# Optimization experiments

Measured on AMD Instinct MI355X. Metric: run time of the kernel, lower is better.

The kernel has to match this reference:

```python
import jax, jax.numpy as jnp
import numpy as np
from jax import lax

K = 3  # conv kernel size (causal)

def causal_conv1d(x, w, b):
    # x: [B, T, Cin], w: [K, Cin, Cout], b: [Cout]
    # TF 'causal' padding = pad left with (K-1) zeros.
    y = lax.conv_general_dilated(
        x, w,
        window_strides=(1,),
        padding=[(K - 1, 0)],
        dimension_numbers=("NWC", "WIO", "NWC"),
    )
    return y + b

def setup_inputs() -> dict:
    key = jax.random.key(0)
    ks = jax.random.split(key, 7)
    B, T, Cin, U = 8, 2048, 512, 512
    scale_in = 1.0 / np.sqrt(K * Cin)
    x = jax.random.normal(ks[0], (B, T, Cin), dtype=jnp.float32)
    Wq = jax.random.normal(ks[1], (K, Cin, U), dtype=jnp.float32) * scale_in
    Wk = jax.random.normal(ks[2], (K, Cin, U), dtype=jnp.float32) * scale_in
    Wv = jax.random.normal(ks[3], (K, Cin, U), dtype=jnp.float32) * scale_in
    bq = jnp.zeros((U,), dtype=jnp.float32)
    bk = jnp.zeros((U,), dtype=jnp.float32)
    bv = jnp.zeros((U,), dtype=jnp.float32)
    return {"x": x, "Wq": Wq, "bq": bq, "Wk": Wk, "bk": bk, "Wv": Wv, "bv": bv}

def reference(x, Wq, bq, Wk, bk, Wv, bv):
    # Self-attention path: query = key = value = x
    q = causal_conv1d(x, Wq, bq)   # [B, T, U]
    k = causal_conv1d(x, Wk, bk)   # [B, T, U]
    v = causal_conv1d(x, Wv, bv)   # [B, T, U]
    score = jnp.einsum("bqd,bkd->bqk", q, k)
    score = score / jnp.sqrt(jnp.asarray(v.shape[-1], dtype=score.dtype))
    # NOTE: faithful to source — softmax over axis=1 (the QUERY axis)
    score = jax.nn.softmax(score, axis=1)
    context = jnp.einsum("bqk,bkd->bqd", score, v)  # [B, T, U]
    return context
```

## Files before the change

### kernel.cpp

```cpp
#include <hip/hip_runtime.h>


#define B_   8
#define T_   2048
#define D_   512
#define KC_  1536
#define TPAD_ 2050

using short8   = __attribute__((ext_vector_type(8))) short;
using float4v  = __attribute__((ext_vector_type(4))) float;

__device__ __forceinline__ float bf2f(unsigned short b) {
  unsigned u = ((unsigned)b) << 16;
  float f; __builtin_memcpy(&f, &u, 4); return f;
}
__device__ __forceinline__ unsigned short f2bf(float f) {
  unsigned u; __builtin_memcpy(&u, &f, 4);
  u += 0x7fffu + ((u >> 16) & 1u);
  return (unsigned short)(u >> 16);
}

__device__ __forceinline__ void gld16(const void* g, void* l) {
  __builtin_amdgcn_global_load_lds((__attribute__((address_space(1))) void*)g,
                                   (__attribute__((address_space(3))) void*)l,
                                   16, 0, 0);
}

__device__ __forceinline__ float4v mfma16(short8 a, short8 b, float4v c) {
  return __builtin_amdgcn_mfma_f32_16x16x32_bf16(a, b, c, 0, 0, 0);
}

__global__ __launch_bounds__(256) void prep_x(const float* __restrict__ x,
                                              unsigned short* __restrict__ xpad) {
  const int b = blockIdx.y;
  const int i = (blockIdx.x * 256 + threadIdx.x) * 4;
  const int t = i >> 9;
  unsigned short* dst = xpad + (size_t)b * (TPAD_ * D_) + i;
  if (t < 2) {
    dst[0] = 0; dst[1] = 0; dst[2] = 0; dst[3] = 0;
  } else {
    const float* sp = x + ((size_t)b * T_ + (t - 2)) * D_ + (i & 511);
    float4v v = *(const float4v*)sp;
    dst[0] = f2bf(v[0]); dst[1] = f2bf(v[1]); dst[2] = f2bf(v[2]); dst[3] = f2bf(v[3]);
  }
}

__global__ __launch_bounds__(256) void transpose_w3(const float* __restrict__ Wq,
                                                    const float* __restrict__ Wk,
                                                    const float* __restrict__ Wv,
                                                    unsigned short* __restrict__ Wt,
                                                    const float* __restrict__ bq,
                                                    const float* __restrict__ bk,
                                                    const float* __restrict__ bv,
                                                    float* __restrict__ bcat) {
  __shared__ unsigned short tile[64][65];
  const float* s = (blockIdx.z == 0) ? Wq : (blockIdx.z == 1) ? Wk : Wv;
  unsigned short* d = Wt + (size_t)blockIdx.z * D_ * KC_;
  const int r0 = blockIdx.x * 64, c0 = blockIdx.y * 64;
  const int tc = threadIdx.x & 63, tg = threadIdx.x >> 6;
  if (blockIdx.x == 0 && blockIdx.y == 0) {
    const float* bsrc = (blockIdx.z == 0) ? bq : (blockIdx.z == 1) ? bk : bv;
    bcat[blockIdx.z * 512 + threadIdx.x] = bsrc[threadIdx.x];
    bcat[blockIdx.z * 512 + 256 + threadIdx.x] = bsrc[256 + threadIdx.x];
  }
#pragma unroll
  for (int i = 0; i < 16; i++) {
    const int r = i * 4 + tg;
    tile[r][tc] = f2bf(s[(size_t)(r0 + r) * D_ + (c0 + tc)]);
  }
  __syncthreads();
#pragma unroll
  for (int i = 0; i < 16; i++) {
    const int rr = i * 4 + tg;
    d[(size_t)(c0 + rr) * KC_ + (r0 + tc)] = tile[tc][rr];
  }
}

__global__ __launch_bounds__(256) void transpose_v(const unsigned short* __restrict__ src,
                                                   unsigned short* __restrict__ dst) {
  __shared__ unsigned short tile[64][65];
  const unsigned short* s = src + (size_t)blockIdx.z * T_ * KC_;
  unsigned short* d = dst + (size_t)blockIdx.z * D_ * T_;
  const int r0 = blockIdx.x * 64, c0 = blockIdx.y * 64;
  const int tc = threadIdx.x & 63, tg = threadIdx.x >> 6;
#pragma unroll
  for (int i = 0; i < 16; i++) {
    const int r = i * 4 + tg;
    tile[r][tc] = s[(size_t)(r0 + r) * KC_ + (c0 + tc)];
  }
  __syncthreads();
#pragma unroll
  for (int i = 0; i < 16; i++) {
    const int rr = i * 4 + tg;
    d[(size_t)(c0 + rr) * T_ + (r0 + tc)] = tile[tc][rr];
  }
}

__global__ __launch_bounds__(256) void scale_vt2(unsigned short* __restrict__ Vt,
                                                 long long sVz,
                                                 const float* __restrict__ pl,
                                                 long long sPz) {
  const size_t z = blockIdx.z;
  unsigned short* Vb = Vt + z * (size_t)sVz;
  const float* Lz = pl + z * (size_t)sPz;
  const int k0 = threadIdx.x * 8;
  float4v a = *(const float4v*)(Lz + k0);
  float4v b = *(const float4v*)(Lz + k0 + 4);
  float inv[8];
#pragma unroll
  for (int j = 0; j < 4; j++) { inv[j] = 1.f / a[j]; inv[4 + j] = 1.f / b[j]; }
  const int d0 = blockIdx.x * 8;
#pragma unroll
  for (int r = 0; r < 8; r++) {
    unsigned short* p = Vb + (size_t)(d0 + r) * T_ + k0;
    short8 v = *(const short8*)p;
    short8 o;
#pragma unroll
    for (int j = 0; j < 8; j++)
      o[j] = (short)f2bf(bf2f((unsigned short)v[j]) * inv[j]);
    *(short8*)p = o;
  }
}


#define RD_A(MH, BUF)                                                        \
  {                                                                          \
    const unsigned short* p_ =                                               \
        lds + (BUF) * 8192 + aoff + (MH) * (HFA * 1024);                     \
    _Pragma("unroll") for (int f_ = 0; f_ < HFA; ++f_) {                     \
      afr[MH][f_][0] = *(const short8*)(p_ + f_ * 1024 + q0);                \
      afr[MH][f_][1] = *(const short8*)(p_ + f_ * 1024 + q1);                \
    }                                                                        \
  }

#define RD_B(NH, BUF)                                                        \
  {                                                                          \
    const unsigned short* p_ =                                               \
        lds + 16384 + (BUF) * BLD + boff + (NH) * (HFB * 1024);              \
    _Pragma("unroll") for (int f_ = 0; f_ < HFB; ++f_) {                     \
      bfr[NH][f_][0] = *(const short8*)(p_ + f_ * 1024 + q0);                \
      bfr[NH][f_][1] = *(const short8*)(p_ + f_ * 1024 + q1);                \
    }                                                                        \
  }

#define MMA(MH, NH)                                                          \
  __builtin_amdgcn_s_setprio(1);                                             \
  _Pragma("unroll") for (int s_ = 0; s_ < 2; ++s_)                           \
  _Pragma("unroll") for (int f_ = 0; f_ < HFA; ++f_)                         \
  _Pragma("unroll") for (int g_ = 0; g_ < HFB; ++g_)                         \
      acc[(MH) * HFA + f_][(NH) * HFB + g_] =                                \
          mfma16(afr[MH][f_][s_], bfr[NH][g_][s_],                           \
                 acc[(MH) * HFA + f_][(NH) * HFB + g_]);                     \
  __builtin_amdgcn_s_setprio(0);

#define PH_MID                                                               \
  __builtin_amdgcn_s_barrier();                                              \
  asm volatile("s_waitcnt lgkmcnt(0)" ::: "memory");                         \
  __builtin_amdgcn_sched_barrier(0);

#define PH_END __builtin_amdgcn_s_barrier();

#define VMW                                                                  \
  do {                                                                       \
    if constexpr (GB == 6)                                                   \
      asm volatile("s_waitcnt vmcnt(6)" ::: "memory");                       \
    else                                                                     \
      asm volatile("s_waitcnt vmcnt(4)" ::: "memory");                       \
  } while (0)

template <int MODE, int BN>
__global__ __launch_bounds__(256, 2)
void gemm8(const unsigned short* __restrict__ A, long long sAz, int lda,
           const unsigned short* __restrict__ Bm, long long sBz, int ldb,
           void* __restrict__ Out, long long sOz, int ldo,
           const float* __restrict__ bias,
           float* __restrict__ pl, long long sPz,
           int Kdim, float scale) {
  constexpr int RW  = 64;
  constexpr int CW  = BN / 2;
  constexpr int FA  = 4;
  constexpr int FB  = CW / 16;
  constexpr int HFA = 2;
  constexpr int HFB = FB / 2;
  constexpr int GB  = BN / 32;
  constexpr int GBP2 = GB / 2;
  constexpr int BLD = BN * 64;
  __shared__ unsigned short lds[16384 + 2 * BLD];

  const int tid = threadIdx.x;
  const int l = tid & 63;
  const int wv = tid >> 6;
  const int wm = wv >> 1, wn = wv & 1;
  const int l15 = l & 15, hi = l >> 4, l7 = l & 7;
  const size_t z = blockIdx.z;
  const unsigned short* Ab = A + z * (size_t)sAz;
  const unsigned short* Bb = Bm + z * (size_t)sBz;
  const int m0 = blockIdx.x * 128, n0 = blockIdx.y * BN;
  const int NT = Kdim >> 6;
  const int NIT = NT >> 1;

  const int srow = tid >> 3;
  const int cswz = ((tid & 7) ^ ((tid >> 3) & 7)) << 3;
  const unsigned short* gA = Ab + (size_t)(m0 + srow) * lda + cswz;
  const unsigned short* gB = Bb + (size_t)(n0 + srow) * ldb + cswz;

  auto stgA = [&](int buf, int h, int kt) {
    if (kt >= NT) kt = NT - 1;
    unsigned short* d = lds + buf * 8192 + h * 4096 + tid * 8;
    const unsigned short* g = gA + (size_t)(h * 64) * lda + kt * 64;
    gld16(g, d);
    gld16(g + (size_t)32 * lda, d + 2048);
  };
  auto stgB = [&](int buf, int g, int kt) {
    if (kt >= NT) kt = NT - 1;
    unsigned short* d = lds + 16384 + buf * BLD + g * 2048 + tid * 8;
    const unsigned short* gp = gB + (size_t)(g * 32) * ldb + kt * 64;
    gld16(gp, d);
  };

  const int aoff = (wm * RW + l15) * 64;
  const int boff = (wn * CW + l15) * 64;
  const int q0 = ((0 + hi) ^ l7) << 3;
  const int q1 = ((4 + hi) ^ l7) << 3;

  short8 afr[2][HFA][2];
  short8 bfr[2][HFB][2];
  float4v acc[FA][FB];
#pragma unroll
  for (int i = 0; i < FA; ++i)
#pragma unroll
    for (int j = 0; j < FB; ++j)
#pragma unroll
      for (int r = 0; r < 4; ++r) acc[i][j][r] = 0.f;

#pragma unroll
  for (int g = 0; g < GB; ++g) stgB(0, g, 0);
  stgA(0, 0, 0); stgA(0, 1, 0);
#pragma unroll
  for (int g = 0; g < GB; ++g) stgB(1, g, 1);
  VMW;
  __builtin_amdgcn_s_barrier();
  __builtin_amdgcn_sched_barrier(0);

  for (int it = 0; it < NIT; ++it) {
    const int kt = 2 * it;
    RD_A(0, 0); RD_B(0, 0);
    stgA(1, 0, kt + 1);
    PH_MID; MMA(0, 0); PH_END;
    RD_B(1, 0);
    stgA(1, 1, kt + 1);
    PH_MID; MMA(0, 1); PH_END;
    RD_A(1, 0);
#pragma unroll
    for (int g = 0; g < GBP2; ++g) stgB(0, g, kt + 2);
    PH_MID; MMA(1, 1); PH_END;
#pragma unroll
    for (int g = GBP2; g < GB; ++g) stgB(0, g, kt + 2);
    PH_MID; MMA(1, 0); VMW; PH_END;
    RD_A(0, 1); RD_B(0, 1);
    stgA(0, 0, kt + 2);
    PH_MID; MMA(0, 0); PH_END;
    RD_B(1, 1);
    stgA(0, 1, kt + 2);
    PH_MID; MMA(0, 1); PH_END;
    RD_A(1, 1);
#pragma unroll
    for (int g = 0; g < GBP2; ++g) stgB(1, g, kt + 3);
    PH_MID; MMA(1, 1); PH_END;
#pragma unroll
    for (int g = GBP2; g < GB; ++g) stgB(1, g, kt + 3);
    PH_MID; MMA(1, 0); VMW; PH_END;
  }

  const int r0 = m0 + wm * RW + hi * 4;
  const int c0 = n0 + wn * CW + l15;

  if constexpr (MODE == 2) {
    float* O = (float*)Out + z * (size_t)sOz;
#pragma unroll
    for (int fm = 0; fm < FA; ++fm)
#pragma unroll
      for (int fn = 0; fn < FB; ++fn)
#pragma unroll
        for (int r = 0; r < 4; ++r)
          O[(size_t)(r0 + fm * 16 + r) * ldo + (c0 + fn * 16)] =
              acc[fm][fn][r] * scale;
  } else if constexpr (MODE == 0) {
    unsigned short* O = (unsigned short*)Out + z * (size_t)sOz;
#pragma unroll
    for (int fn = 0; fn < FB; ++fn) {
      const float badd = bias[c0 + fn * 16];
#pragma unroll
      for (int fm = 0; fm < FA; ++fm)
#pragma unroll
        for (int r = 0; r < 4; ++r)
          O[(size_t)(r0 + fm * 16 + r) * ldo + (c0 + fn * 16)] =
              f2bf(acc[fm][fn][r] * scale + badd);
    }
  } else {
    unsigned short* O = (unsigned short*)Out + z * (size_t)sOz;
    float cs[FB];
#pragma unroll
    for (int fn = 0; fn < FB; ++fn) cs[fn] = 0.f;
#pragma unroll
    for (int fm = 0; fm < FA; ++fm)
#pragma unroll
      for (int fn = 0; fn < FB; ++fn)
#pragma unroll
        for (int r = 0; r < 4; ++r) {
          float e = __expf(acc[fm][fn][r] * scale - 16.f);
          cs[fn] += e;
          O[(size_t)(r0 + fm * 16 + r) * ldo + (c0 + fn * 16)] = f2bf(e);
        }
#pragma unroll
    for (int fn = 0; fn < FB; ++fn) {
      cs[fn] += __shfl_xor(cs[fn], 16, 64);
      cs[fn] += __shfl_xor(cs[fn], 32, 64);
    }
    if (hi == 0) {
#pragma unroll
      for (int fn = 0; fn < FB; ++fn)
        atomicAdd(&pl[z * (size_t)sPz + (c0 + fn * 16)], cs[fn]);
    }
  }
}

extern "C" void kernel_launch(void* const* d_in, const int* in_sizes, int n_in,
                              void* d_out, int out_size, void* d_ws, size_t ws_size,
                              hipStream_t stream) {
  const float* x  = (const float*)d_in[0];
  const float* Wq = (const float*)d_in[1];
  const float* bq = (const float*)d_in[2];
  const float* Wk = (const float*)d_in[3];
  const float* bk = (const float*)d_in[4];
  const float* Wv = (const float*)d_in[5];
  const float* bv = (const float*)d_in[6];

  char* ws = (char*)d_ws;
  auto alloc = [&](size_t bytes) {
    char* p = ws; ws += (bytes + 255) & ~(size_t)255; return p;
  };
  unsigned short* xpad = (unsigned short*)alloc((size_t)B_ * TPAD_ * D_ * 2);
  unsigned short* Wt   = (unsigned short*)alloc((size_t)KC_ * KC_ * 2);
  float*          bcat = (float*)alloc((size_t)KC_ * 4);
  unsigned short* QKV  = (unsigned short*)alloc((size_t)B_ * T_ * KC_ * 2);
  unsigned short* Vt   = (unsigned short*)alloc((size_t)B_ * D_ * T_ * 2);
  float* pl   = (float*)alloc((size_t)B_ * T_ * 4);
  size_t used = (size_t)(ws - (char*)d_ws);
  const size_t sAll = (size_t)B_ * T_ * T_ * 2;
  const size_t sOne = (size_t)T_ * T_ * 2;
  const int NB = (used + sAll <= ws_size) ? B_ : 1;
  unsigned short* Sb = (unsigned short*)alloc(NB == B_ ? sAll : sOne);

  hipMemsetAsync(pl, 0, (size_t)B_ * T_ * 4, stream);
  prep_x<<<dim3(1025, B_), 256, 0, stream>>>(x, xpad);
  transpose_w3<<<dim3(24, 8, 3), 256, 0, stream>>>(Wq, Wk, Wv, Wt,
                                                   bq, bk, bv, bcat);

  gemm8<0, 192><<<dim3(16, 8, B_), 256, 0, stream>>>(
      xpad, (long long)TPAD_ * D_, D_,
      Wt, 0, KC_,
      QKV, (long long)T_ * KC_, KC_,
      bcat, nullptr, 0, KC_, 1.0f);

  transpose_v<<<dim3(32, 8, B_), 256, 0, stream>>>(QKV + 2 * D_, Vt);

  const float scale = 0.044194173824159216f;
  for (int b0 = 0; b0 < B_; b0 += NB) {
    const unsigned short* Qp = QKV + (size_t)b0 * T_ * KC_;
    const unsigned short* Kp = QKV + (size_t)b0 * T_ * KC_ + D_;
    gemm8<1, 128><<<dim3(16, 16, NB), 256, 0, stream>>>(
        Qp, (long long)T_ * KC_, KC_,
        Kp, (long long)T_ * KC_, KC_,
        Sb, (long long)T_ * T_, T_,
        nullptr, pl + (size_t)b0 * T_, (long long)T_,
        D_, scale);
    scale_vt2<<<dim3(64, 1, NB), 256, 0, stream>>>(
        Vt + (size_t)b0 * D_ * T_, (long long)D_ * T_,
        pl + (size_t)b0 * T_, (long long)T_);
    gemm8<2, 128><<<dim3(16, 4, NB), 256, 0, stream>>>(
        Sb, (long long)T_ * T_, T_,
        Vt + (size_t)b0 * D_ * T_, (long long)D_ * T_, T_,
        (float*)d_out + (size_t)b0 * T_ * D_, (long long)T_ * D_, D_,
        nullptr, nullptr, 0, T_, 1.0f);
  }
}
```

Before: 254.4 us.

## Fuse V transpose with softmax scaling and coarsen GEMM main-loop phases

Merges the V transpose kernel and the separate per-column softmax scaling kernel into one kernel that scales each element by the reciprocal column sum while writing the transposed tile. This removes one full read-modify-write pass over Vt and one launch. It also restructures the gemm8 main loop from four MMA phases per k-tile to two, issuing more LDS reads and global stages before each larger MMA batch. That trades finer interleaving of loads and compute for fewer phase barriers, and raises register pressure.

```diff
diff --git a/kernel.cpp b/kernel.cpp
--- a/kernel.cpp
+++ b/kernel.cpp
@@ -76,11 +76,14 @@
   }
 }
 
-__global__ __launch_bounds__(256) void transpose_v(const unsigned short* __restrict__ src,
-                                                   unsigned short* __restrict__ dst) {
+__global__ __launch_bounds__(256) void transpose_scale_v(
+    const unsigned short* __restrict__ src, const unsigned short* __restrict__,
+    unsigned short* __restrict__ dst, long long sVz,
+    const float* __restrict__ pl, long long sPz) {
   __shared__ unsigned short tile[64][65];
-  const unsigned short* s = src + (size_t)blockIdx.z * T_ * KC_;
-  unsigned short* d = dst + (size_t)blockIdx.z * D_ * T_;
+  const size_t z = blockIdx.z;
+  const unsigned short* s = src + z * (size_t)T_ * KC_;
+  unsigned short* d = dst + z * (size_t)sVz;
   const int r0 = blockIdx.x * 64, c0 = blockIdx.y * 64;
   const int tc = threadIdx.x & 63, tg = threadIdx.x >> 6;
 #pragma unroll
@@ -88,37 +91,13 @@
     const int r = i * 4 + tg;
     tile[r][tc] = s[(size_t)(r0 + r) * KC_ + (c0 + tc)];
   }
+  const float myinv = 1.0f / pl[z * (size_t)sPz + (r0 + tc)];
   __syncthreads();
 #pragma unroll
   for (int i = 0; i < 16; i++) {
     const int rr = i * 4 + tg;
-    d[(size_t)(c0 + rr) * T_ + (r0 + tc)] = tile[tc][rr];
-  }
-}
-
-__global__ __launch_bounds__(256) void scale_vt2(unsigned short* __restrict__ Vt,
-                                                 long long sVz,
-                                                 const float* __restrict__ pl,
-                                                 long long sPz) {
-  const size_t z = blockIdx.z;
-  unsigned short* Vb = Vt + z * (size_t)sVz;
-  const float* Lz = pl + z * (size_t)sPz;
-  const int k0 = threadIdx.x * 8;
-  float4v a = *(const float4v*)(Lz + k0);
-  float4v b = *(const float4v*)(Lz + k0 + 4);
-  float inv[8];
-#pragma unroll
-  for (int j = 0; j < 4; j++) { inv[j] = 1.f / a[j]; inv[4 + j] = 1.f / b[j]; }
-  const int d0 = blockIdx.x * 8;
-#pragma unroll
-  for (int r = 0; r < 8; r++) {
-    unsigned short* p = Vb + (size_t)(d0 + r) * T_ + k0;
-    short8 v = *(const short8*)p;
-    short8 o;
-#pragma unroll
-    for (int j = 0; j < 8; j++)
-      o[j] = (short)f2bf(bf2f((unsigned short)v[j]) * inv[j]);
-    *(short8*)p = o;
+    d[(size_t)(c0 + rr) * T_ + (r0 + tc)] =
+        f2bf(bf2f(tile[tc][rr]) * myinv);
   }
 }
 
@@ -183,7 +162,6 @@
   constexpr int HFA = 2;
   constexpr int HFB = FB / 2;
   constexpr int GB  = BN / 32;
-  constexpr int GBP2 = GB / 2;
   constexpr int BLD = BN * 64;
   __shared__ unsigned short lds[16384 + 2 * BLD];
 
@@ -244,32 +222,20 @@
 
   for (int it = 0; it < NIT; ++it) {
     const int kt = 2 * it;
-    RD_A(0, 0); RD_B(0, 0);
-    stgA(1, 0, kt + 1);
-    PH_MID; MMA(0, 0); PH_END;
-    RD_B(1, 0);
-    stgA(1, 1, kt + 1);
-    PH_MID; MMA(0, 1); PH_END;
+    RD_A(0, 0); RD_B(0, 0); RD_B(1, 0);
+    stgA(1, 0, kt + 1); stgA(1, 1, kt + 1);
+    PH_MID; MMA(0, 0); MMA(0, 1); PH_END;
     RD_A(1, 0);
 #pragma unroll
-    for (int g = 0; g < GBP2; ++g) stgB(0, g, kt + 2);
-    PH_MID; MMA(1, 1); PH_END;
-#pragma unroll
-    for (int g = GBP2; g < GB; ++g) stgB(0, g, kt + 2);
-    PH_MID; MMA(1, 0); VMW; PH_END;
-    RD_A(0, 1); RD_B(0, 1);
-    stgA(0, 0, kt + 2);
-    PH_MID; MMA(0, 0); PH_END;
-    RD_B(1, 1);
-    stgA(0, 1, kt + 2);
-    PH_MID; MMA(0, 1); PH_END;
+    for (int g = 0; g < GB; ++g) stgB(0, g, kt + 2);
+    PH_MID; MMA(1, 1); MMA(1, 0); VMW; PH_END;
+    RD_A(0, 1); RD_B(0, 1); RD_B(1, 1);
+    stgA(0, 0, kt + 2); stgA(0, 1, kt + 2);
+    PH_MID; MMA(0, 0); MMA(0, 1); PH_END;
     RD_A(1, 1);
 #pragma unroll
-    for (int g = 0; g < GBP2; ++g) stgB(1, g, kt + 3);
-    PH_MID; MMA(1, 1); PH_END;
-#pragma unroll
-    for (int g = GBP2; g < GB; ++g) stgB(1, g, kt + 3);
-    PH_MID; MMA(1, 0); VMW; PH_END;
+    for (int g = 0; g < GB; ++g) stgB(1, g, kt + 3);
+    PH_MID; MMA(1, 1); MMA(1, 0); VMW; PH_END;
   }
 
   const int r0 = m0 + wm * RW + hi * 4;
@@ -363,8 +329,6 @@
       QKV, (long long)T_ * KC_, KC_,
       bcat, nullptr, 0, KC_, 1.0f);
 
-  transpose_v<<<dim3(32, 8, B_), 256, 0, stream>>>(QKV + 2 * D_, Vt);
-
   const float scale = 0.044194173824159216f;
   for (int b0 = 0; b0 < B_; b0 += NB) {
     const unsigned short* Qp = QKV + (size_t)b0 * T_ * KC_;
@@ -375,7 +339,8 @@
         Sb, (long long)T_ * T_, T_,
         nullptr, pl + (size_t)b0 * T_, (long long)T_,
         D_, scale);
-    scale_vt2<<<dim3(64, 1, NB), 256, 0, stream>>>(
+    transpose_scale_v<<<dim3(32, 8, NB), 256, 0, stream>>>(
+        QKV + (size_t)b0 * T_ * KC_ + 2 * D_, nullptr,
         Vt + (size_t)b0 * D_ * T_, (long long)D_ * T_,
         pl + (size_t)b0 * T_, (long long)T_);
     gemm8<2, 128><<<dim3(16, 4, NB), 256, 0, stream>>>(
```

Result: no change. 258.9 us (+1.8%).
